# Kernel tuning notes

Hardware: AMD Instinct MI355X
Metric: run time of the kernel (lower is better)

Reference implementation:

```python
import jax, jax.numpy as jnp
import numpy as np

K = 20          # neighbors
BN_EPS = 1e-5


def _knn_idx(x, k):
    """x: [B, C, N] -> idx of k nearest neighbors [B, N, k] (by squared distance, self included)."""
    xx = jnp.sum(x * x, axis=1)                       # [B, N]
    inner = jnp.einsum('bcn,bcm->bnm', x, x)          # [B, N, N]
    neg_sqdist = 2.0 * inner - xx[:, :, None] - xx[:, None, :]
    return jax.lax.top_k(neg_sqdist, k)[1]            # [B, N, k]


def _graph_feature(x, k):
    """x: [B, C, N] -> edge features cat(x_j - x_i, x_i): [B, 2C, N, k]."""
    idx = _knn_idx(x, k)                              # [B, N, k]
    xT = x.transpose(0, 2, 1)                         # [B, N, C]
    nbrs = jax.vmap(lambda xt, ii: xt[ii])(xT, idx)   # [B, N, k, C] gather
    center = xT[:, :, None, :]                        # [B, N, 1, C]
    feat = jnp.concatenate(
        [nbrs - center, jnp.broadcast_to(center, nbrs.shape)], axis=-1)  # [B, N, k, 2C]
    return feat.transpose(0, 3, 1, 2)                 # [B, 2C, N, k]


def _conv_bn_lrelu(feat, W, gamma, beta, mean, var):
    """1x1 Conv2d (no bias) + BatchNorm (given stats) + LeakyReLU(0.2). feat: [B, Cin, N, k]."""
    y = jnp.einsum('oc,bcnk->bonk', W, feat)
    scale = (gamma / jnp.sqrt(var + BN_EPS))[None, :, None, None]
    y = (y - mean[None, :, None, None]) * scale + beta[None, :, None, None]
    return jnp.where(y > 0, y, 0.2 * y)


def setup_inputs() -> dict:
    key = jax.random.key(0)
    ks = list(jax.random.split(key, 32))
    B, N = 8, 1024
    f32 = jnp.float32

    def w(kk, o, i):
        return jax.random.normal(kk, (o, i), dtype=f32) / np.sqrt(i)

    def bn(k1, k2, k3, k4, c):
        g = jax.random.uniform(k1, (c,), dtype=f32, minval=0.5, maxval=1.5)
        b = jax.random.normal(k2, (c,), dtype=f32) * 0.05
        m = jax.random.normal(k3, (c,), dtype=f32) * 0.05
        v = jax.random.uniform(k4, (c,), dtype=f32, minval=0.5, maxval=1.5)
        return g, b, m, v

    x = jax.random.normal(ks[0], (B, N, 3), dtype=f32)
    W0 = w(ks[1], 64, 6);    g0, b0, m0, v0 = bn(ks[2], ks[3], ks[4], ks[5], 64)
    W1 = w(ks[6], 128, 128); g1, b1, m1, v1 = bn(ks[7], ks[8], ks[9], ks[10], 128)
    W2 = w(ks[11], 256, 256); g2, b2, m2, v2 = bn(ks[12], ks[13], ks[14], ks[15], 256)
    Wf = w(ks[16], 512, 896); gf, bf, mf, vf = bn(ks[17], ks[18], ks[19], ks[20], 512)
    We = w(ks[21], 256, 512)
    return dict(x=x,
                W0=W0, g0=g0, b0=b0, m0=m0, v0=v0,
                W1=W1, g1=g1, b1=b1, m1=m1, v1=v1,
                W2=W2, g2=g2, b2=b2, m2=m2, v2=v2,
                Wf=Wf, gf=gf, bf=bf, mf=mf, vf=vf,
                We=We)


def reference(x, W0, g0, b0, m0, v0, W1, g1, b1, m1, v1,
              W2, g2, b2, m2, v2, Wf, gf, bf, mf, vf, We):
    h = x.transpose(0, 2, 1)                          # [B, 3, N]
    outs = []
    for (W, g, b, m, v) in ((W0, g0, b0, m0, v0),
                            (W1, g1, b1, m1, v1),
                            (W2, g2, b2, m2, v2)):
        gfeat = _graph_feature(h, K)                  # [B, 2C, N, k]
        y = _conv_bn_lrelu(gfeat, W, g, b, m, v)      # [B, Cout, N, k]
        h = y.mean(axis=-1)                           # max-free EdgeConv pool over k
        outs.append(h)
    cat = jnp.concatenate(outs, axis=1)               # [B, 448, N]
    gfeat = _graph_feature(cat, K)                    # [B, 896, N, k]
    y = _conv_bn_lrelu(gfeat, Wf, gf, bf, mf, vf)     # [B, 512, N, k]
    pooled = y.mean(axis=-1).mean(axis=-1)            # [B, 512] (pool over k then N)
    return pooled @ We.T                              # [B, num_features]
```

## Files before the change

### kernel.cpp

```cpp
#include <hip/hip_runtime.h>
#include <cstdint>

#define KNN 20
#define BV 8
#define NV 1024

template <int CTRL>
__device__ __forceinline__ float dppmaxf(float x) {
    int xi = __float_as_int(x);
    int mi = __builtin_amdgcn_update_dpp(xi, xi, CTRL, 0xf, 0xf, false);
    return fmaxf(x, __int_as_float(mi));
}
template <int CTRL>
__device__ __forceinline__ unsigned dppmin(unsigned x) {
    unsigned m = (unsigned)__builtin_amdgcn_update_dpp((int)x, (int)x, CTRL, 0xf, 0xf, false);
    return (x < m) ? x : m;
}
__device__ __forceinline__ float wave_max_f32(float x) {
    x = dppmaxf<0xB1>(x); x = dppmaxf<0x4E>(x); x = dppmaxf<0x141>(x);
    x = dppmaxf<0x140>(x); x = dppmaxf<0x142>(x); x = dppmaxf<0x143>(x);
    return __int_as_float(__builtin_amdgcn_readlane(__float_as_int(x), 63));
}
__device__ __forceinline__ unsigned wave_min_u32(unsigned x) {
    x = dppmin<0xB1>(x); x = dppmin<0x4E>(x); x = dppmin<0x141>(x);
    x = dppmin<0x140>(x); x = dppmin<0x142>(x); x = dppmin<0x143>(x);
    return (unsigned)__builtin_amdgcn_readlane((int)x, 63);
}

__global__ __launch_bounds__(256) void k_transpose(const float* __restrict__ x, float* __restrict__ hx) {
    int id = blockIdx.x * 256 + threadIdx.x;
    if (id >= BV * 3 * NV) return;
    int n = id % NV;
    int c = (id / NV) % 3;
    int b = id / (3 * NV);
    hx[id] = x[(b * NV + n) * 3 + c];
}

__global__ __launch_bounds__(256) void k_xx(const float* __restrict__ h, float* __restrict__ xx,
                                            int C, int bstride) {
    int id = blockIdx.x * 256 + threadIdx.x;
    int n = id % NV, b = id / NV;
    if (b >= BV) return;
    const float* hp = h + (size_t)b * bstride + n;
    float s = 0.f;
    for (int c = 0; c < C; ++c) { float v = hp[(size_t)c * NV]; s += v * v; }
    xx[b * NV + n] = s;
}

__global__ __launch_bounds__(512, 2) void k_knn(const float* __restrict__ h, const float* __restrict__ xx,
                                                int C, int bstride, int* __restrict__ idx) {
    __shared__ float Bs[8][1024];
    __shared__ float sv[16][2][KNN];
    __shared__ int   sj[16][2][KNN];
    const int bx = blockIdx.x;
    const int b = bx & 7, tile = bx >> 3;
    const int i0 = tile * 16;
    const int t = threadIdx.x, lane = t & 63, w = t >> 6;
    const int rg = w & 3, hf = w >> 2;
    const int irow = i0 + rg * 4;
    const int jb = hf * 512;
    float acc[4][8] = {};
    const float* hb = h + (size_t)b * bstride;

    for (int c0 = 0; c0 < C; c0 += 8) {
        __syncthreads();
#pragma unroll
        for (int r = 0; r < 4; ++r) {
            int e = r * 512 + t;
            int cc = e >> 8, jj = e & 255;
            float4 v = make_float4(0.f, 0.f, 0.f, 0.f);
            if (c0 + cc < C) v = *(const float4*)&hb[(size_t)(c0 + cc) * NV + jj * 4];
            *(float4*)&Bs[cc][jj * 4] = v;
        }
        __syncthreads();
#pragma unroll
        for (int c = 0; c < 8; ++c) {
            float4 arv = *(const float4*)&Bs[c][irow];
            float ar[4] = {arv.x, arv.y, arv.z, arv.w};
            float br[8];
#pragma unroll
            for (int g = 0; g < 2; ++g) {
                float4 bv = *(const float4*)&Bs[c][jb + g * 256 + (lane << 2)];
                br[g * 4 + 0] = bv.x; br[g * 4 + 1] = bv.y;
                br[g * 4 + 2] = bv.z; br[g * 4 + 3] = bv.w;
            }
#pragma unroll
            for (int a = 0; a < 4; ++a)
#pragma unroll
                for (int q = 0; q < 8; ++q) acc[a][q] += ar[a] * br[q];
        }
    }

    const float* xb = xx + b * NV;
    float xxj[8];
#pragma unroll
    for (int g = 0; g < 2; ++g) {
        float4 xv = *(const float4*)&xb[jb + g * 256 + (lane << 2)];
        xxj[g * 4 + 0] = xv.x; xxj[g * 4 + 1] = xv.y;
        xxj[g * 4 + 2] = xv.z; xxj[g * 4 + 3] = xv.w;
    }
#pragma unroll
    for (int a = 0; a < 4; ++a) {
        float xi = xb[irow + a];
#pragma unroll
        for (int q = 0; q < 8; ++q) acc[a][q] = 2.f * acc[a][q] - xi - xxj[q];
    }

#pragma unroll 1
    for (int s = 0; s < KNN; ++s) {
#pragma unroll
        for (int a = 0; a < 4; ++a) {
            float w0[4]; int p0[4];
#pragma unroll
            for (int i = 0; i < 4; ++i) {
                bool g = acc[a][2 * i + 1] > acc[a][2 * i];
                w0[i] = g ? acc[a][2 * i + 1] : acc[a][2 * i];
                p0[i] = g ? 2 * i + 1 : 2 * i;
            }
            float w1[2]; int p1[2];
#pragma unroll
            for (int i = 0; i < 2; ++i) {
                bool g = w0[2 * i + 1] > w0[2 * i];
                w1[i] = g ? w0[2 * i + 1] : w0[2 * i];
                p1[i] = g ? p0[2 * i + 1] : p0[2 * i];
            }
            bool gf = w1[1] > w1[0];
            float bv = gf ? w1[1] : w1[0];
            int bq = gf ? p1[1] : p1[0];

            float gmax = wave_max_f32(bv);
            int myj = jb + ((bq >> 2) << 8) + (lane << 2) + (bq & 3);
            unsigned cand = (bv == gmax) ? (unsigned)myj : 0xFFFFFFFFu;
            int j = (int)wave_min_u32(cand);
            if (lane == 0) {
                sv[rg * 4 + a][hf][s] = gmax;
                sj[rg * 4 + a][hf][s] = j;
            }
            int wq = (cand == (unsigned)j) ? bq : 99;
#pragma unroll
            for (int q = 0; q < 8; ++q)
                if (wq == q) acc[a][q] = -3.4e38f;
        }
    }

    __syncthreads();
    if (t < 16) {
        const float* v0 = sv[t][0];
        const float* v1 = sv[t][1];
        const int* j0 = sj[t][0];
        const int* j1 = sj[t][1];
        int* op = idx + ((size_t)(b * NV + i0 + t)) * KNN;
        int a = 0, c2 = 0;
#pragma unroll
        for (int s = 0; s < KNN; ++s) {
            float va = v0[a], vb = v1[c2];
            int ja = j0[a], jb2 = j1[c2];
            bool take0 = (va > vb) || (va == vb && ja < jb2);
            op[s] = take0 ? ja : jb2;
            a += take0 ? 1 : 0;
            c2 += take0 ? 0 : 1;
        }
    }
}

__global__ __launch_bounds__(256) void k_pack(const float* __restrict__ W, float* __restrict__ wb,
                                              int C, int O) {
    int id = blockIdx.x * 256 + threadIdx.x;
    if (id >= 2 * O * C) return;
    int c = id % C, o = (id / C) % O, half = id / (C * O);
    float wl = W[(size_t)o * 2 * C + c];
    wb[id] = half ? (W[(size_t)o * 2 * C + C + c] - wl) : wl;
}

__global__ __launch_bounds__(256) void k_gemm(const float* __restrict__ A, int astride,
                                              const float* __restrict__ h, int bstride, int C,
                                              float* __restrict__ out, int O) {
    __shared__ float Ws[8][64], Hs[8][128];
    const int b = blockIdx.x, n0 = blockIdx.y * 128, o0 = blockIdx.z * 64;
    const int t = threadIdx.x, tx = t & 15, ty = t >> 4;
    float acc[4][8] = {};
    const float* hb = h + (size_t)b * bstride;
    for (int c0 = 0; c0 < C; c0 += 8) {
#pragma unroll
        for (int q = 0; q < 2; ++q) {
            int e = t + q * 256;
            int oo = e >> 3, cc = e & 7;
            Ws[cc][oo] = ((c0 + cc) < C) ? A[(size_t)(o0 + oo) * astride + c0 + cc] : 0.f;
        }
        {
            int cc = t >> 5, nn4 = t & 31;
            float4 v = make_float4(0.f, 0.f, 0.f, 0.f);
            if (c0 + cc < C) v = *(const float4*)&hb[(size_t)(c0 + cc) * NV + n0 + nn4 * 4];
            *(float4*)&Hs[cc][nn4 * 4] = v;
        }
        __syncthreads();
#pragma unroll
        for (int c = 0; c < 8; ++c) {
            float4 wv = *(const float4*)&Ws[c][ty * 4];
            float ar[4] = {wv.x, wv.y, wv.z, wv.w};
            float br[8];
            float4 h0 = *(const float4*)&Hs[c][tx * 4];
            float4 h1 = *(const float4*)&Hs[c][64 + tx * 4];
            br[0] = h0.x; br[1] = h0.y; br[2] = h0.z; br[3] = h0.w;
            br[4] = h1.x; br[5] = h1.y; br[6] = h1.z; br[7] = h1.w;
#pragma unroll
            for (int a = 0; a < 4; ++a)
#pragma unroll
                for (int q = 0; q < 8; ++q) acc[a][q] += ar[a] * br[q];
        }
        __syncthreads();
    }
#pragma unroll
    for (int a = 0; a < 4; ++a) {
        int o = o0 + ty * 4 + a;
        float* outp = out + ((size_t)b * O + o) * NV + n0;
        float4 s0 = make_float4(acc[a][0], acc[a][1], acc[a][2], acc[a][3]);
        float4 s1 = make_float4(acc[a][4], acc[a][5], acc[a][6], acc[a][7]);
        *(float4*)&outp[tx * 4] = s0;
        *(float4*)&outp[64 + tx * 4] = s1;
    }
}

__global__ __launch_bounds__(256) void k_edge(const float* __restrict__ pd,
                                              const int* __restrict__ idx,
                                              const float* __restrict__ ga, const float* __restrict__ be,
                                              const float* __restrict__ mu, const float* __restrict__ va,
                                              float* __restrict__ out, int out_bstride, int O) {
    const int b = blockIdx.x;
    const int n = blockIdx.y * 256 + threadIdx.x;
    const int o0 = blockIdx.z * 4;
    const int* ip = idx + ((size_t)b * NV + n) * KNN;
    int jj[KNN];
#pragma unroll
    for (int k = 0; k < KNN; ++k) jj[k] = ip[k];
#pragma unroll
    for (int a = 0; a < 4; ++a) {
        const int o = o0 + a;
        const float al = ga[o] / sqrtf(va[o] + 1e-5f);
        const float c0 = be[o] - mu[o] * al;
        const float* pb = pd + ((size_t)b * 2 * O + o) * NV;
        const float dv  = pd[((size_t)b * 2 * O + O + o) * NV + n];
        float s = 0.f;
#pragma unroll
        for (int k = 0; k < KNN; ++k) {
            float y = fmaf(al, pb[jj[k]] + dv, c0);
            s += (y > 0.f) ? y : 0.2f * y;
        }
        out[(size_t)b * out_bstride + (size_t)o * NV + n] = s * (1.f / KNN);
    }
}

__global__ __launch_bounds__(256) void k_pool(const float* __restrict__ hf, float* __restrict__ pooled) {
    const int o = blockIdx.x, b = blockIdx.y;
    const float* hp = hf + ((size_t)b * 512 + o) * NV;
    float s = 0.f;
    for (int i = threadIdx.x; i < NV; i += 256) s += hp[i];
#pragma unroll
    for (int off = 32; off > 0; off >>= 1) s += __shfl_down(s, off, 64);
    __shared__ float red[4];
    if ((threadIdx.x & 63) == 0) red[threadIdx.x >> 6] = s;
    __syncthreads();
    if (threadIdx.x == 0)
        pooled[(size_t)b * 512 + o] = (red[0] + red[1] + red[2] + red[3]) * (1.f / NV);
}

__global__ __launch_bounds__(256) void k_final(const float* __restrict__ pooled, const float* __restrict__ We,
                                               float* __restrict__ out) {
    const int j = threadIdx.x, b = blockIdx.x;
    __shared__ float ps[512];
    for (int o = threadIdx.x; o < 512; o += 256) ps[o] = pooled[b * 512 + o];
    __syncthreads();
    float s = 0.f;
    for (int o = 0; o < 512; ++o) s += ps[o] * We[(size_t)j * 512 + o];
    out[b * 256 + j] = s;
}

extern "C" void kernel_launch(void* const* d_in, const int* in_sizes, int n_in,
                              void* d_out, int out_size, void* d_ws, size_t ws_size,
                              hipStream_t stream) {
    const float* x  = (const float*)d_in[0];
    const float* W0 = (const float*)d_in[1];
    const float* g0 = (const float*)d_in[2];
    const float* b0 = (const float*)d_in[3];
    const float* m0 = (const float*)d_in[4];
    const float* v0 = (const float*)d_in[5];
    const float* W1 = (const float*)d_in[6];
    const float* g1 = (const float*)d_in[7];
    const float* b1 = (const float*)d_in[8];
    const float* m1 = (const float*)d_in[9];
    const float* v1 = (const float*)d_in[10];
    const float* W2 = (const float*)d_in[11];
    const float* g2 = (const float*)d_in[12];
    const float* b2 = (const float*)d_in[13];
    const float* m2 = (const float*)d_in[14];
    const float* v2 = (const float*)d_in[15];
    const float* Wf = (const float*)d_in[16];
    const float* gf = (const float*)d_in[17];
    const float* bf = (const float*)d_in[18];
    const float* mf = (const float*)d_in[19];
    const float* vf = (const float*)d_in[20];
    const float* We = (const float*)d_in[21];

    float* ws = (float*)d_ws;
    float* hx     = ws;
    float* cat    = hx + 24576;
    float* xx     = cat + 3670016;
    int*   idx    = (int*)(xx + 8192);
    float* pd     = (float*)(idx + 163840);
    float* wb     = pd + 8388608;
    float* hf     = wb + 458752;
    float* pooled = hf + 4194304;

    k_transpose<<<96, 256, 0, stream>>>(x, hx);

    auto run_layer = [&](const float* h, int C, int bstride, const float* W,
                         const float* g, const float* be, const float* m, const float* v,
                         int O, float* outp, int obstride) {
        k_xx<<<32, 256, 0, stream>>>(h, xx, C, bstride);
        k_knn<<<512, 512, 0, stream>>>(h, xx, C, bstride, idx);
        int pn = 2 * O * C;
        k_pack<<<(pn + 255) / 256, 256, 0, stream>>>(W, wb, C, O);
        k_gemm<<<dim3(8, 8, 2 * O / 64), 256, 0, stream>>>(wb, C, h, bstride, C, pd, 2 * O);
        k_edge<<<dim3(8, 4, O / 4), 256, 0, stream>>>(pd, idx, g, be, m, v, outp, obstride, O);
    };

    run_layer(hx, 3, 3 * NV, W0, g0, b0, m0, v0, 64, cat, 448 * NV);
    run_layer(cat, 64, 448 * NV, W1, g1, b1, m1, v1, 128, cat + 64 * NV, 448 * NV);
    run_layer(cat + 64 * NV, 128, 448 * NV, W2, g2, b2, m2, v2, 256, cat + 192 * NV, 448 * NV);
    run_layer(cat, 448, 448 * NV, Wf, gf, bf, mf, vf, 512, hf, 512 * NV);

    k_pool<<<dim3(512, 8), 256, 0, stream>>>(hf, pooled);
    k_final<<<8, 256, 0, stream>>>(pooled, We, (float*)d_out);
}
```

Before: 846.0 us.

## Add full-row kNN variant, fold weight packing into GEMM load, read A rows from global

Result: slower. 1.062 ms (+25.5%).

```diff
diff --git a/kernel.cpp b/kernel.cpp
--- a/kernel.cpp
+++ b/kernel.cpp
@@ -47,8 +47,111 @@
     xx[b * NV + n] = s;
 }
 
-__global__ __launch_bounds__(512, 2) void k_knn(const float* __restrict__ h, const float* __restrict__ xx,
-                                                int C, int bstride, int* __restrict__ idx) {
+__global__ __launch_bounds__(512, 2) void k_knnF(const float* __restrict__ h, const float* __restrict__ xx,
+                                                 int C, int bstride, int* __restrict__ idx) {
+    __shared__ float Bs[8][1024];
+    const int bx = blockIdx.x;
+    const int b = bx & 7, tile = bx >> 3;
+    const int i0 = tile * 16;
+    const int t = threadIdx.x, lane = t & 63, w = t >> 6;
+    const int irow = i0 + w * 2;
+    float acc[2][16] = {};
+    const float* hb = h + (size_t)b * bstride;
+
+    for (int c0 = 0; c0 < C; c0 += 8) {
+        __syncthreads();
+#pragma unroll
+        for (int r = 0; r < 4; ++r) {
+            int e = r * 512 + t;
+            int cc = e >> 8, jj = e & 255;
+            float4 v = make_float4(0.f, 0.f, 0.f, 0.f);
+            if (c0 + cc < C) v = *(const float4*)&hb[(size_t)(c0 + cc) * NV + jj * 4];
+            *(float4*)&Bs[cc][jj * 4] = v;
+        }
+        float2 ar2[8];
+#pragma unroll
+        for (int cc = 0; cc < 8; ++cc) {
+            ar2[cc] = make_float2(0.f, 0.f);
+            if (c0 + cc < C) ar2[cc] = *(const float2*)&hb[(size_t)(c0 + cc) * NV + irow];
+        }
+        __syncthreads();
+#pragma unroll
+        for (int c = 0; c < 8; ++c) {
+            float ar[2] = {ar2[c].x, ar2[c].y};
+            float br[16];
+#pragma unroll
+            for (int g = 0; g < 4; ++g) {
+                float4 bv = *(const float4*)&Bs[c][g * 256 + (lane << 2)];
+                br[g * 4 + 0] = bv.x; br[g * 4 + 1] = bv.y;
+                br[g * 4 + 2] = bv.z; br[g * 4 + 3] = bv.w;
+            }
+#pragma unroll
+            for (int a = 0; a < 2; ++a)
+#pragma unroll
+                for (int q = 0; q < 16; ++q) acc[a][q] += ar[a] * br[q];
+        }
+    }
+
+    const float* xb = xx + b * NV;
+    float xxj[16];
+#pragma unroll
+    for (int g = 0; g < 4; ++g) {
+        float4 xv = *(const float4*)&xb[g * 256 + (lane << 2)];
+        xxj[g * 4 + 0] = xv.x; xxj[g * 4 + 1] = xv.y;
+        xxj[g * 4 + 2] = xv.z; xxj[g * 4 + 3] = xv.w;
+    }
+#pragma unroll
+    for (int a = 0; a < 2; ++a) {
+        float xi = xb[irow + a];
+#pragma unroll
+        for (int q = 0; q < 16; ++q) acc[a][q] = 2.f * acc[a][q] - xi - xxj[q];
+    }
+
+    int* opb = idx + ((size_t)(b * NV + irow)) * KNN;
+#pragma unroll 1
+    for (int s = 0; s < KNN; ++s) {
+#pragma unroll
+        for (int a = 0; a < 2; ++a) {
+            float w0[8]; int p0[8];
+#pragma unroll
+            for (int i = 0; i < 8; ++i) {
+                bool g = acc[a][2 * i + 1] > acc[a][2 * i];
+                w0[i] = g ? acc[a][2 * i + 1] : acc[a][2 * i];
+                p0[i] = g ? 2 * i + 1 : 2 * i;
+            }
+            float w1[4]; int p1[4];
+#pragma unroll
+            for (int i = 0; i < 4; ++i) {
+                bool g = w0[2 * i + 1] > w0[2 * i];
+                w1[i] = g ? w0[2 * i + 1] : w0[2 * i];
+                p1[i] = g ? p0[2 * i + 1] : p0[2 * i];
+            }
+            float w2[2]; int p2[2];
+#pragma unroll
+            for (int i = 0; i < 2; ++i) {
+                bool g = w1[2 * i + 1] > w1[2 * i];
+                w2[i] = g ? w1[2 * i + 1] : w1[2 * i];
+                p2[i] = g ? p1[2 * i + 1] : p1[2 * i];
+            }
+            bool gf = w2[1] > w2[0];
+            float bv = gf ? w2[1] : w2[0];
+            int bq = gf ? p2[1] : p2[0];
+
+            float gmax = wave_max_f32(bv);
+            int myj = ((bq >> 2) << 8) + (lane << 2) + (bq & 3);
+            unsigned cand = (bv == gmax) ? (unsigned)myj : 0xFFFFFFFFu;
+            int j = (int)wave_min_u32(cand);
+            if (lane == 0) opb[a * KNN + s] = j;
+            int wq = (cand == (unsigned)j) ? bq : 99;
+#pragma unroll
+            for (int q = 0; q < 16; ++q)
+                if (wq == q) acc[a][q] = -3.4e38f;
+        }
+    }
+}
+
+__global__ __launch_bounds__(512, 2) void k_knnS(const float* __restrict__ h, const float* __restrict__ xx,
+                                                 int C, int bstride, int* __restrict__ idx) {
     __shared__ float Bs[8][1024];
     __shared__ float sv[16][2][KNN];
     __shared__ int   sj[16][2][KNN];
@@ -72,11 +175,16 @@
             if (c0 + cc < C) v = *(const float4*)&hb[(size_t)(c0 + cc) * NV + jj * 4];
             *(float4*)&Bs[cc][jj * 4] = v;
         }
+        float4 ar8[8];
+#pragma unroll
+        for (int cc = 0; cc < 8; ++cc) {
+            ar8[cc] = make_float4(0.f, 0.f, 0.f, 0.f);
+            if (c0 + cc < C) ar8[cc] = *(const float4*)&hb[(size_t)(c0 + cc) * NV + irow];
+        }
         __syncthreads();
 #pragma unroll
         for (int c = 0; c < 8; ++c) {
-            float4 arv = *(const float4*)&Bs[c][irow];
-            float ar[4] = {arv.x, arv.y, arv.z, arv.w};
+            float ar[4] = {ar8[c].x, ar8[c].y, ar8[c].z, ar8[c].w};
             float br[8];
 #pragma unroll
             for (int g = 0; g < 2; ++g) {
@@ -163,18 +271,9 @@
     }
 }
 
-__global__ __launch_bounds__(256) void k_pack(const float* __restrict__ W, float* __restrict__ wb,
-                                              int C, int O) {
-    int id = blockIdx.x * 256 + threadIdx.x;
-    if (id >= 2 * O * C) return;
-    int c = id % C, o = (id / C) % O, half = id / (C * O);
-    float wl = W[(size_t)o * 2 * C + c];
-    wb[id] = half ? (W[(size_t)o * 2 * C + C + c] - wl) : wl;
-}
-
-__global__ __launch_bounds__(256) void k_gemm(const float* __restrict__ A, int astride,
+__global__ __launch_bounds__(256) void k_gemm(const float* __restrict__ W, int O,
                                               const float* __restrict__ h, int bstride, int C,
-                                              float* __restrict__ out, int O) {
+                                              float* __restrict__ out) {
     __shared__ float Ws[8][64], Hs[8][128];
     const int b = blockIdx.x, n0 = blockIdx.y * 128, o0 = blockIdx.z * 64;
     const int t = threadIdx.x, tx = t & 15, ty = t >> 4;
@@ -185,7 +284,17 @@
         for (int q = 0; q < 2; ++q) {
             int e = t + q * 256;
             int oo = e >> 3, cc = e & 7;
-            Ws[cc][oo] = ((c0 + cc) < C) ? A[(size_t)(o0 + oo) * astride + c0 + cc] : 0.f;
+            int r = o0 + oo;
+            float v = 0.f;
+            if (c0 + cc < C) {
+                if (r < O) {
+                    v = W[(size_t)r * 2 * C + c0 + cc];
+                } else {
+                    const float* wr = W + (size_t)(r - O) * 2 * C;
+                    v = wr[C + c0 + cc] - wr[c0 + cc];
+                }
+            }
+            Ws[cc][oo] = v;
         }
         {
             int cc = t >> 5, nn4 = t & 31;
@@ -213,7 +322,7 @@
 #pragma unroll
     for (int a = 0; a < 4; ++a) {
         int o = o0 + ty * 4 + a;
-        float* outp = out + ((size_t)b * O + o) * NV + n0;
+        float* outp = out + ((size_t)b * 2 * O + o) * NV + n0;
         float4 s0 = make_float4(acc[a][0], acc[a][1], acc[a][2], acc[a][3]);
         float4 s1 = make_float4(acc[a][4], acc[a][5], acc[a][6], acc[a][7]);
         *(float4*)&outp[tx * 4] = s0;
@@ -307,27 +416,27 @@
     float* xx     = cat + 3670016;
     int*   idx    = (int*)(xx + 8192);
     float* pd     = (float*)(idx + 163840);
-    float* wb     = pd + 8388608;
-    float* hf     = wb + 458752;
+    float* hf     = pd + 8388608;
     float* pooled = hf + 4194304;
 
     k_transpose<<<96, 256, 0, stream>>>(x, hx);
 
     auto run_layer = [&](const float* h, int C, int bstride, const float* W,
                          const float* g, const float* be, const float* m, const float* v,
-                         int O, float* outp, int obstride) {
+                         int O, float* outp, int obstride, bool jsplit) {
         k_xx<<<32, 256, 0, stream>>>(h, xx, C, bstride);
-        k_knn<<<512, 512, 0, stream>>>(h, xx, C, bstride, idx);
-        int pn = 2 * O * C;
-        k_pack<<<(pn + 255) / 256, 256, 0, stream>>>(W, wb, C, O);
-        k_gemm<<<dim3(8, 8, 2 * O / 64), 256, 0, stream>>>(wb, C, h, bstride, C, pd, 2 * O);
+        if (jsplit)
+            k_knnS<<<512, 512, 0, stream>>>(h, xx, C, bstride, idx);
+        else
+            k_knnF<<<512, 512, 0, stream>>>(h, xx, C, bstride, idx);
+        k_gemm<<<dim3(8, 8, 2 * O / 64), 256, 0, stream>>>(W, O, h, bstride, C, pd);
         k_edge<<<dim3(8, 4, O / 4), 256, 0, stream>>>(pd, idx, g, be, m, v, outp, obstride, O);
     };
 
-    run_layer(hx, 3, 3 * NV, W0, g0, b0, m0, v0, 64, cat, 448 * NV);
-    run_layer(cat, 64, 448 * NV, W1, g1, b1, m1, v1, 128, cat + 64 * NV, 448 * NV);
-    run_layer(cat + 64 * NV, 128, 448 * NV, W2, g2, b2, m2, v2, 256, cat + 192 * NV, 448 * NV);
-    run_layer(cat, 448, 448 * NV, Wf, gf, bf, mf, vf, 512, hf, 512 * NV);
+    run_layer(hx, 3, 3 * NV, W0, g0, b0, m0, v0, 64, cat, 448 * NV, false);
+    run_layer(cat, 64, 448 * NV, W1, g1, b1, m1, v1, 128, cat + 64 * NV, 448 * NV, false);
+    run_layer(cat + 64 * NV, 128, 448 * NV, W2, g2, b2, m2, v2, 256, cat + 192 * NV, 448 * NV, false);
+    run_layer(cat, 448, 448 * NV, Wf, gf, bf, mf, vf, 512, hf, 512 * NV, true);
 
     k_pool<<<dim3(512, 8), 256, 0, stream>>>(hf, pooled);
     k_final<<<8, 256, 0, stream>>>(pooled, We, (float*)d_out);
```
